# Kernel tuning notes

Hardware: AMD Instinct MI355X
Metric: run time of the kernel (lower is better)

The kernel has to match this reference:

```python
import jax, jax.numpy as jnp
import numpy as np

NODE_DIM, EDGE_DIM, HIDDEN, OUT_DIM, HEADS = 128, 64, 128, 64, 4
N_NODES, N_EDGES = 4096, 16384
EPS = 1e-8


def setup_inputs() -> dict:
    key = jax.random.key(0)
    ks = jax.random.split(key, 10)
    s = lambda *shape: 1.0 / np.sqrt(shape[-2] if len(shape) > 1 else shape[-1])
    return {
        "node_features": jax.random.normal(ks[0], (N_NODES, NODE_DIM), jnp.float32),
        "incidence_matrix": jax.random.uniform(ks[1], (N_NODES, N_EDGES), jnp.float32),
        # per-head node_transform: [H, node_dim, hidden]
        "W1": jax.random.normal(ks[2], (HEADS, NODE_DIM, HIDDEN), jnp.float32) * (1.0 / np.sqrt(NODE_DIM)),
        "b1": jnp.zeros((HEADS, HIDDEN), jnp.float32),
        # per-head attention_weight: Linear(hidden, 1) -> vector [H, hidden]
        "Wa": jax.random.normal(ks[3], (HEADS, HIDDEN), jnp.float32) * (1.0 / np.sqrt(HIDDEN)),
        "ba": jnp.zeros((HEADS,), jnp.float32),
        # per-head expand_output: [H, hidden, edge_dim]
        "W2": jax.random.normal(ks[4], (HEADS, HIDDEN, EDGE_DIM), jnp.float32) * (1.0 / np.sqrt(HIDDEN)),
        "b2": jnp.zeros((HEADS, EDGE_DIM), jnp.float32),
        # output_transform: [H*edge_dim, output_dim]
        "Wout": jax.random.normal(ks[5], (HEADS * EDGE_DIM, OUT_DIM), jnp.float32) * (1.0 / np.sqrt(HEADS * EDGE_DIM)),
        "bout": jnp.zeros((OUT_DIM,), jnp.float32),
    }


def _min_max_normalize(x):
    # per-column min-max over the edge axis (axis=-2)
    mn = jnp.min(x, axis=-2, keepdims=True)
    mx = jnp.max(x, axis=-2, keepdims=True)
    return (x - mn) / (mx - mn + EPS)


def reference(node_features, incidence_matrix, W1, b1, Wa, ba, W2, b2, Wout, bout):
    # transformed node features per head: [H, N, hidden]
    t = jnp.einsum("nd,hdk->hnk", node_features, W1) + b1[:, None, :]
    # incidence^T @ t -> masked edge features: [H, E, hidden]
    m = jnp.einsum("ne,hnk->hek", incidence_matrix, t)
    # attention scores: [H, E]
    scores = jnp.einsum("hek,hk->he", m, Wa) + ba[:, None]
    scores = jax.nn.leaky_relu(scores, negative_slope=0.2)
    # softmax over edges (dim=0 of [E,1] per head)
    coeffs = jax.nn.softmax(scores, axis=-1)  # [H, E]
    w = coeffs[:, :, None] * m  # [H, E, hidden]
    u = jnp.einsum("hek,hko->heo", w, W2) + b2[:, None, :]  # [H, E, edge_dim]
    u = _min_max_normalize(u)
    # concat heads -> [E, H*edge_dim]
    cat = jnp.transpose(u, (1, 0, 2)).reshape(N_EDGES, HEADS * EDGE_DIM)
    cat = jax.nn.relu(cat)  # dropout is identity in eval mode
    return cat @ Wout + bout  # [E, output_dim]
```

## Files before the change

### kernel.cpp

```cpp
#include <hip/hip_runtime.h>
#include <stdint.h>

#define NODES 4096
#define EDGES 16384
#define CSTR  288

typedef __attribute__((ext_vector_type(4))) float    f32x4;
typedef __attribute__((ext_vector_type(8))) short    short8;
typedef __attribute__((ext_vector_type(4))) uint32_t u32x4;
typedef __attribute__((ext_vector_type(4))) unsigned short u16x4;

__device__ __forceinline__ unsigned short f2bf(float f) {
  union { float f; uint32_t u; } v; v.f = f;
  uint32_t u = v.u;
  return (unsigned short)((u + 0x7fffu + ((u >> 16) & 1u)) >> 16);
}
__device__ __forceinline__ float bf2f(unsigned short s) {
  union { uint32_t u; float f; } v; v.u = ((uint32_t)s) << 16;
  return v.f;
}
__device__ __forceinline__ uint32_t fenc(float f) {
  uint32_t u = __float_as_uint(f);
  return (u >> 31) ? ~u : (u | 0x80000000u);
}
__device__ __forceinline__ float fdec(uint32_t k) {
  return (k & 0x80000000u) ? __uint_as_float(k ^ 0x80000000u) : __uint_as_float(~k);
}

__global__ __launch_bounds__(128) void k0_fold(
    const float* __restrict__ W1, const float* __restrict__ W2,
    const float* __restrict__ Wa, const float* __restrict__ b1,
    float* __restrict__ WeT, float* __restrict__ beff)
{
  const int h = blockIdx.x / 65, oi = blockIdx.x % 65;
  const int d = threadIdx.x;
  const float* W1r = W1 + (size_t)h * 16384 + (size_t)d * 128;
  float acc = 0.f, p;
  if (oi < 64) {
    const float* w2c = W2 + (size_t)h * 8192 + oi;
#pragma unroll 8
    for (int kc = 0; kc < 32; kc++) {
      f32x4 wv = *(const f32x4*)(W1r + kc * 4);
      acc += wv[0] * w2c[(size_t)(kc * 4 + 0) * 64];
      acc += wv[1] * w2c[(size_t)(kc * 4 + 1) * 64];
      acc += wv[2] * w2c[(size_t)(kc * 4 + 2) * 64];
      acc += wv[3] * w2c[(size_t)(kc * 4 + 3) * 64];
    }
    p = b1[h * 128 + d] * w2c[(size_t)d * 64];
  } else {
    const float* wac = Wa + h * 128;
#pragma unroll 8
    for (int kc = 0; kc < 32; kc++) {
      f32x4 wv = *(const f32x4*)(W1r + kc * 4);
      f32x4 av = *(const f32x4*)(wac + kc * 4);
      acc += wv[0] * av[0] + wv[1] * av[1] + wv[2] * av[2] + wv[3] * av[3];
    }
    p = b1[h * 128 + d] * wac[d];
  }
  WeT[(size_t)h * 9216 + (size_t)d * 72 + oi] = acc;
  for (int off = 32; off > 0; off >>= 1) p += __shfl_down(p, off, 64);
  __shared__ float r2s[2];
  if ((d & 63) == 0) r2s[d >> 6] = p;
  __syncthreads();
  if (d == 0) beff[h * 72 + oi] = r2s[0] + r2s[1];
}

__global__ __launch_bounds__(256) void k1_prep(
    const float* __restrict__ nf, const float* __restrict__ WeT,
    const float* __restrict__ beff, unsigned short* __restrict__ PqT)
{
  __shared__ float nf_s[8][132];
  const int n0 = blockIdx.x * 8;
  const int t = threadIdx.x;
  {
    int row = t >> 5, col = (t * 4) & 127;
    *(f32x4*)&nf_s[row][col] = *(const f32x4*)(nf + (size_t)(n0 + row) * 128 + col);
  }
  __syncthreads();
  const int h = t >> 6, o = t & 63;
  const float* wp = WeT + (size_t)h * 9216 + o;
  float acc[8];
  {
    float b = beff[h * 72 + o];
#pragma unroll
    for (int n = 0; n < 8; n++) acc[n] = b;
  }
  for (int dc = 0; dc < 32; dc++) {
    f32x4 nv[8];
#pragma unroll
    for (int n = 0; n < 8; n++) nv[n] = *(const f32x4*)&nf_s[n][dc * 4];
#pragma unroll
    for (int i = 0; i < 4; i++) {
      float wv = wp[(size_t)(dc * 4 + i) * 72];
#pragma unroll
      for (int n = 0; n < 8; n++) acc[n] += nv[n][i] * wv;
    }
  }
  {
    unsigned short b[8];
#pragma unroll
    for (int n = 0; n < 8; n++) b[n] = f2bf(acc[n]);
    u32x4 pk;
    pk[0] = (uint32_t)b[0] | ((uint32_t)b[1] << 16);
    pk[1] = (uint32_t)b[2] | ((uint32_t)b[3] << 16);
    pk[2] = (uint32_t)b[4] | ((uint32_t)b[5] << 16);
    pk[3] = (uint32_t)b[6] | ((uint32_t)b[7] << 16);
    *(u32x4*)(&PqT[(size_t)(h * 72 + o) * 4096 + n0]) = pk;
  }
  if (t < 32) {
    const int qh = t >> 3, qn = t & 7;
    const float* wq = WeT + (size_t)qh * 9216 + 64;
    float a = beff[qh * 72 + 64];
    for (int d = 0; d < 128; d++) a += nf_s[qn][d] * wq[(size_t)d * 72];
    unsigned short hi = f2bf(a);
    unsigned short lo = f2bf(a - bf2f(hi));
    PqT[(size_t)(qh * 72 + 64) * 4096 + n0 + qn] = hi;
    PqT[(size_t)(qh * 72 + 65) * 4096 + n0 + qn] = lo;
  }
  if (t < 96) {
    const int ph = t / 24, pr = (t / 4) % 6, pn = (t & 3) * 2;
    *(uint32_t*)&PqT[(size_t)(ph * 72 + 66 + pr) * 4096 + n0 + pn] = 0u;
  }
}

__global__ __launch_bounds__(256) void k2_gemm(
    const float* __restrict__ inc, const unsigned short* __restrict__ PqT,
    float* __restrict__ C, float* __restrict__ sbuf)
{
  __shared__ unsigned short As[64 * 64];
  __shared__ unsigned short AsLo[64 * 64];
  __shared__ unsigned short Bs[288 * 72];
  const int t = threadIdx.x;
  const int lane = t & 63, w = t >> 6;
  const int wr = w & 1, wc = w >> 1;
  const int e0 = blockIdx.x * 64;
  const int eq = t & 15, kq = t >> 4;

  f32x4 acc[2][9];
  for (int mi = 0; mi < 2; mi++)
    for (int ni = 0; ni < 9; ni++)
      acc[mi][ni] = (f32x4){0.f, 0.f, 0.f, 0.f};

  f32x4 av[4];
  u32x4 bv[9];

  auto load_tiles = [&](int ks) {
    const float* ap = inc + (size_t)(ks * 64 + kq * 4) * 16384 + e0 + eq * 4;
#pragma unroll
    for (int r = 0; r < 4; r++)
      av[r] = *(const f32x4*)(ap + (size_t)r * 16384);
#pragma unroll
    for (int j = 0; j < 9; j++) {
      int f = t + 256 * j; int c = f >> 3, q8 = f & 7;
      bv[j] = *(const u32x4*)(PqT + (size_t)c * 4096 + ks * 64 + q8 * 8);
    }
  };
  auto store_tiles = [&]() {
#pragma unroll
    for (int i = 0; i < 4; i++) {
      int e = 4 * eq + i;
      int p = ((kq >> 1) + eq + 4 * i) & 7;
      u16x4 wv, wl;
      wv[0] = f2bf(av[0][i]); wv[1] = f2bf(av[1][i]);
      wv[2] = f2bf(av[2][i]); wv[3] = f2bf(av[3][i]);
      wl[0] = f2bf(av[0][i] - bf2f(wv[0]));
      wl[1] = f2bf(av[1][i] - bf2f(wv[1]));
      wl[2] = f2bf(av[2][i] - bf2f(wv[2]));
      wl[3] = f2bf(av[3][i] - bf2f(wv[3]));
      *(u16x4*)(&As[e * 64 + p * 8 + (kq & 1) * 4]) = wv;
      *(u16x4*)(&AsLo[e * 64 + p * 8 + (kq & 1) * 4]) = wl;
    }
#pragma unroll
    for (int j = 0; j < 9; j++) {
      int f = t + 256 * j; int c = f >> 3, q8 = f & 7;
      *(u32x4*)(&Bs[c * 72 + q8 * 8]) = bv[j];
    }
  };
  auto compute = [&]() {
#pragma unroll
    for (int ksub = 0; ksub < 2; ksub++) {
      short8 afr[2], aflo[2];
      const int q = lane >> 4;
#pragma unroll
      for (int mi = 0; mi < 2; mi++) {
        int e = wr * 32 + mi * 16 + (lane & 15);
        int p = ((4 * ksub + q) + (e >> 2) + 4 * (e & 3)) & 7;
        afr[mi]  = *(const short8*)(&As[e * 64 + p * 8]);
        aflo[mi] = *(const short8*)(&AsLo[e * 64 + p * 8]);
      }
#pragma unroll
      for (int ni = 0; ni < 9; ni++) {
        int c = wc * 144 + ni * 16 + (lane & 15);
        const short8 bfr = *(const short8*)(&Bs[c * 72 + 32 * ksub + 8 * q]);
        acc[0][ni] = __builtin_amdgcn_mfma_f32_16x16x32_bf16(afr[0], bfr, acc[0][ni], 0, 0, 0);
        acc[1][ni] = __builtin_amdgcn_mfma_f32_16x16x32_bf16(afr[1], bfr, acc[1][ni], 0, 0, 0);
        if (ni == 4 || ni == 8) {
          acc[0][ni] = __builtin_amdgcn_mfma_f32_16x16x32_bf16(aflo[0], bfr, acc[0][ni], 0, 0, 0);
          acc[1][ni] = __builtin_amdgcn_mfma_f32_16x16x32_bf16(aflo[1], bfr, acc[1][ni], 0, 0, 0);
        }
      }
    }
  };

  load_tiles(0);
  for (int ks = 0; ks < 64; ks++) {
    __syncthreads();
    store_tiles();
    __syncthreads();
    if (ks < 63) load_tiles(ks + 1);
    compute();
  }

#pragma unroll
  for (int mi = 0; mi < 2; mi++)
#pragma unroll
    for (int ni = 0; ni < 9; ni++)
#pragma unroll
      for (int r = 0; r < 4; r++) {
        int e = e0 + wr * 32 + mi * 16 + (lane >> 4) * 4 + r;
        int c = wc * 144 + ni * 16 + (lane & 15);
        C[(size_t)e * CSTR + c] = acc[mi][ni][r];
      }

  const int l15 = lane & 15;
#pragma unroll
  for (int mi = 0; mi < 2; mi++)
#pragma unroll
    for (int r = 0; r < 4; r++) {
      int e = e0 + wr * 32 + mi * 16 + (lane >> 4) * 4 + r;
      {
        float v = acc[mi][4][r]; float vp = __shfl_xor(v, 1);
        if (l15 == 0) sbuf[(wc * 2 + 0) * 16384 + e] = v + vp;
      }
      {
        float v = acc[mi][8][r]; float vp = __shfl_xor(v, 1);
        if (l15 == 8) sbuf[(wc * 2 + 1) * 16384 + e] = v + vp;
      }
    }
}

__global__ __launch_bounds__(1024) void k3_softmax(
    const float* __restrict__ sbuf, const float* __restrict__ ba,
    float* __restrict__ coeff, uint32_t* __restrict__ pmn_a,
    uint32_t* __restrict__ pmx_a)
{
  const int h = blockIdx.x, t = threadIdx.x;
  if (t < 64) { pmn_a[h * 64 + t] = 0xFFFFFFFFu; pmx_a[h * 64 + t] = 0u; }
  __shared__ float red[16];
  float vals[16];
  float mx = -1e30f;
  const float bav = ba[h];
#pragma unroll
  for (int i = 0; i < 16; i++) {
    float s = sbuf[h * 16384 + t + 1024 * i] + bav;
    s = (s > 0.f) ? s : 0.2f * s;
    vals[i] = s;
    mx = fmaxf(mx, s);
  }
  for (int off = 32; off > 0; off >>= 1) mx = fmaxf(mx, __shfl_xor(mx, off, 64));
  if ((t & 63) == 0) red[t >> 6] = mx;
  __syncthreads();
  float gmx = red[0];
  for (int i = 1; i < 16; i++) gmx = fmaxf(gmx, red[i]);
  float total = 0.f;
#pragma unroll
  for (int i = 0; i < 16; i++) { vals[i] = expf(vals[i] - gmx); total += vals[i]; }
  __syncthreads();
  for (int off = 32; off > 0; off >>= 1) total += __shfl_xor(total, off, 64);
  if ((t & 63) == 0) red[t >> 6] = total;
  __syncthreads();
  float gs = 0.f;
  for (int i = 0; i < 16; i++) gs += red[i];
  float inv = 1.f / gs;
#pragma unroll
  for (int i = 0; i < 16; i++) coeff[h * 16384 + t + 1024 * i] = vals[i] * inv;
}

__global__ __launch_bounds__(256) void k4_minmax(
    const float* __restrict__ C, const float* __restrict__ coeff,
    uint32_t* __restrict__ pmn_a, uint32_t* __restrict__ pmx_a)
{
  const int t = threadIdx.x, blk = blockIdx.x;
  const int h = t >> 6, o = t & 63, c = h * 72 + o;
  const int e0 = blk * 64;
  float mn = 1e30f, mx = -1e30f;
  for (int e = 0; e < 64; e++) {
    float u = coeff[h * 16384 + e0 + e] * C[(size_t)(e0 + e) * CSTR + c];
    mn = fminf(mn, u); mx = fmaxf(mx, u);
  }
  atomicMin(&pmn_a[t], fenc(mn));
  atomicMax(&pmx_a[t], fenc(mx));
}

__global__ __launch_bounds__(256) void k5_out(
    const float* __restrict__ C, const float* __restrict__ coeff,
    const uint32_t* __restrict__ pmn_a, const uint32_t* __restrict__ pmx_a,
    const float* __restrict__ Wout, const float* __restrict__ bout,
    float* __restrict__ out)
{
  __shared__ float cat[16][256];
  const int t = threadIdx.x;
  const int e0 = blockIdx.x * 16;
  {
    const int h = t >> 6, o = t & 63, c = h * 72 + o;
    const float mn = fdec(pmn_a[t]);
    const float inv = 1.f / (fdec(pmx_a[t]) - mn + 1e-8f);
#pragma unroll
    for (int el = 0; el < 16; el++) {
      float u = coeff[h * 16384 + e0 + el] * C[(size_t)(e0 + el) * CSTR + c];
      float vn = (u - mn) * inv;
      cat[el][t] = vn > 0.f ? vn : 0.f;
    }
  }
  __syncthreads();
  {
    const int od = t & 63, eg = t >> 6;
    float b = bout[od];
    float a0 = b, a1 = b, a2 = b, a3 = b;
    for (int hc = 0; hc < 256; hc++) {
      float wv = Wout[(size_t)hc * 64 + od];
      a0 += cat[eg * 4 + 0][hc] * wv;
      a1 += cat[eg * 4 + 1][hc] * wv;
      a2 += cat[eg * 4 + 2][hc] * wv;
      a3 += cat[eg * 4 + 3][hc] * wv;
    }
    out[(size_t)(e0 + eg * 4 + 0) * 64 + od] = a0;
    out[(size_t)(e0 + eg * 4 + 1) * 64 + od] = a1;
    out[(size_t)(e0 + eg * 4 + 2) * 64 + od] = a2;
    out[(size_t)(e0 + eg * 4 + 3) * 64 + od] = a3;
  }
}

extern "C" void kernel_launch(void* const* d_in, const int* in_sizes, int n_in,
                              void* d_out, int out_size, void* d_ws, size_t ws_size,
                              hipStream_t stream) {
  const float* nf   = (const float*)d_in[0];
  const float* inc  = (const float*)d_in[1];
  const float* W1   = (const float*)d_in[2];
  const float* b1   = (const float*)d_in[3];
  const float* Wa   = (const float*)d_in[4];
  const float* ba   = (const float*)d_in[5];
  const float* W2   = (const float*)d_in[6];
  const float* Wout = (const float*)d_in[8];
  const float* bout = (const float*)d_in[9];
  float* out = (float*)d_out;

  char* ws = (char*)d_ws;
  unsigned short* PqT = (unsigned short*)(ws);
  float* C      = (float*)(ws + 2359296);
  float* coeff  = (float*)(ws + 21233664);
  float* sbuf   = (float*)(ws + 21495808);
  float* WeT    = (float*)(ws + 21757952);
  float* beff   = (float*)(ws + 21905408);
  uint32_t* pmn_a = (uint32_t*)(ws + 21909504);
  uint32_t* pmx_a = (uint32_t*)(ws + 21910528);

  k0_fold<<<260, 128, 0, stream>>>(W1, W2, Wa, b1, WeT, beff);
  k1_prep<<<512, 256, 0, stream>>>(nf, WeT, beff, PqT);
  k2_gemm<<<256, 256, 0, stream>>>(inc, PqT, C, sbuf);
  k3_softmax<<<4, 1024, 0, stream>>>(sbuf, ba, coeff, pmn_a, pmx_a);
  k4_minmax<<<256, 256, 0, stream>>>(C, coeff, pmn_a, pmx_a);
  k5_out<<<1024, 256, 0, stream>>>(C, coeff, pmn_a, pmx_a, Wout, bout, out);
}
```

Baseline: 464.4 us.

## Store edge features as compact bf16 and run output projection on MFMA

The GEMM epilogue now writes the edge-feature matrix as a dense bf16 [E,256] buffer instead of padded fp32 with stride 288. This cuts the memory traffic of the min-max and output kernels. The output projection is rewritten to use bf16 MFMA over 64-edge tiles, with a bf16 transposed copy of Wout prepared in extra blocks of the fold kernel. The node-prep kernel is reshaped to 128 threads, each computing two output columns. The change adds bf16 rounding error to the intermediate and normalized activations.

```diff
diff --git a/kernel.cpp b/kernel.cpp
--- a/kernel.cpp
+++ b/kernel.cpp
@@ -30,8 +30,24 @@
 __global__ __launch_bounds__(128) void k0_fold(
     const float* __restrict__ W1, const float* __restrict__ W2,
     const float* __restrict__ Wa, const float* __restrict__ b1,
-    float* __restrict__ WeT, float* __restrict__ beff)
-{
+    const float* __restrict__ Wout,
+    float* __restrict__ WeT, float* __restrict__ beff,
+    unsigned short* __restrict__ WoutT)
+{
+  if (blockIdx.x >= 260) {
+    int qi = (blockIdx.x - 260) * 128 + threadIdx.x;
+    if (qi < 4224) {
+      int od = qi / 66, kq = qi % 66;
+      u16x4 v;
+#pragma unroll
+      for (int j = 0; j < 4; j++) {
+        int k = kq * 4 + j;
+        v[j] = (k < 256) ? f2bf(Wout[(size_t)k * 64 + od]) : (unsigned short)0;
+      }
+      *(u16x4*)&WoutT[od * 264 + kq * 4] = v;
+    }
+    return;
+  }
   const int h = blockIdx.x / 65, oi = blockIdx.x % 65;
   const int d = threadIdx.x;
   const float* W1r = W1 + (size_t)h * 16384 + (size_t)d * 128;
@@ -65,25 +81,27 @@
   if (d == 0) beff[h * 72 + oi] = r2s[0] + r2s[1];
 }
 
-__global__ __launch_bounds__(256) void k1_prep(
+__global__ __launch_bounds__(128) void k1_prep(
     const float* __restrict__ nf, const float* __restrict__ WeT,
     const float* __restrict__ beff, unsigned short* __restrict__ PqT)
 {
   __shared__ float nf_s[8][132];
   const int n0 = blockIdx.x * 8;
   const int t = threadIdx.x;
+#pragma unroll
+  for (int i = 0; i < 2; i++) {
+    int idx = t + 128 * i;
+    int row = idx >> 5, c4 = idx & 31;
+    *(f32x4*)&nf_s[row][c4 * 4] = *(const f32x4*)(nf + (size_t)(n0 + row) * 128 + c4 * 4);
+  }
+  __syncthreads();
+  const int h = t >> 5, oo = t & 31;
+  const float* wp = WeT + (size_t)h * 9216 + oo;
+  float acc0[8], acc1[8];
   {
-    int row = t >> 5, col = (t * 4) & 127;
-    *(f32x4*)&nf_s[row][col] = *(const f32x4*)(nf + (size_t)(n0 + row) * 128 + col);
-  }
-  __syncthreads();
-  const int h = t >> 6, o = t & 63;
-  const float* wp = WeT + (size_t)h * 9216 + o;
-  float acc[8];
-  {
-    float b = beff[h * 72 + o];
-#pragma unroll
-    for (int n = 0; n < 8; n++) acc[n] = b;
+    float b0 = beff[h * 72 + oo], b1v = beff[h * 72 + oo + 32];
+#pragma unroll
+    for (int n = 0; n < 8; n++) { acc0[n] = b0; acc1[n] = b1v; }
   }
   for (int dc = 0; dc < 32; dc++) {
     f32x4 nv[8];
@@ -91,21 +109,32 @@
     for (int n = 0; n < 8; n++) nv[n] = *(const f32x4*)&nf_s[n][dc * 4];
 #pragma unroll
     for (int i = 0; i < 4; i++) {
-      float wv = wp[(size_t)(dc * 4 + i) * 72];
-#pragma unroll
-      for (int n = 0; n < 8; n++) acc[n] += nv[n][i] * wv;
+      float w0 = wp[(size_t)(dc * 4 + i) * 72];
+      float w1 = wp[(size_t)(dc * 4 + i) * 72 + 32];
+#pragma unroll
+      for (int n = 0; n < 8; n++) {
+        acc0[n] += nv[n][i] * w0;
+        acc1[n] += nv[n][i] * w1;
+      }
     }
   }
   {
     unsigned short b[8];
 #pragma unroll
-    for (int n = 0; n < 8; n++) b[n] = f2bf(acc[n]);
+    for (int n = 0; n < 8; n++) b[n] = f2bf(acc0[n]);
     u32x4 pk;
     pk[0] = (uint32_t)b[0] | ((uint32_t)b[1] << 16);
     pk[1] = (uint32_t)b[2] | ((uint32_t)b[3] << 16);
     pk[2] = (uint32_t)b[4] | ((uint32_t)b[5] << 16);
     pk[3] = (uint32_t)b[6] | ((uint32_t)b[7] << 16);
-    *(u32x4*)(&PqT[(size_t)(h * 72 + o) * 4096 + n0]) = pk;
+    *(u32x4*)(&PqT[(size_t)(h * 72 + oo) * 4096 + n0]) = pk;
+#pragma unroll
+    for (int n = 0; n < 8; n++) b[n] = f2bf(acc1[n]);
+    pk[0] = (uint32_t)b[0] | ((uint32_t)b[1] << 16);
+    pk[1] = (uint32_t)b[2] | ((uint32_t)b[3] << 16);
+    pk[2] = (uint32_t)b[4] | ((uint32_t)b[5] << 16);
+    pk[3] = (uint32_t)b[6] | ((uint32_t)b[7] << 16);
+    *(u32x4*)(&PqT[(size_t)(h * 72 + oo + 32) * 4096 + n0]) = pk;
   }
   if (t < 32) {
     const int qh = t >> 3, qn = t & 7;
@@ -125,7 +154,7 @@
 
 __global__ __launch_bounds__(256) void k2_gemm(
     const float* __restrict__ inc, const unsigned short* __restrict__ PqT,
-    float* __restrict__ C, float* __restrict__ sbuf)
+    unsigned short* __restrict__ Cb, float* __restrict__ sbuf)
 {
   __shared__ unsigned short As[64 * 64];
   __shared__ unsigned short AsLo[64 * 64];
@@ -214,13 +243,18 @@
 #pragma unroll
   for (int mi = 0; mi < 2; mi++)
 #pragma unroll
-    for (int ni = 0; ni < 9; ni++)
-#pragma unroll
-      for (int r = 0; r < 4; r++) {
-        int e = e0 + wr * 32 + mi * 16 + (lane >> 4) * 4 + r;
-        int c = wc * 144 + ni * 16 + (lane & 15);
-        C[(size_t)e * CSTR + c] = acc[mi][ni][r];
-      }
+    for (int ni = 0; ni < 9; ni++) {
+      int cl = wc * 144 + ni * 16 + (lane & 15);
+      int hl = cl / 72, o = cl - hl * 72;
+      if (o < 64) {
+        int cbcol = hl * 64 + o;
+#pragma unroll
+        for (int r = 0; r < 4; r++) {
+          int e = e0 + wr * 32 + mi * 16 + (lane >> 4) * 4 + r;
+          Cb[(size_t)e * 256 + cbcol] = f2bf(acc[mi][ni][r]);
+        }
+      }
+    }
 
   const int l15 = lane & 15;
 #pragma unroll
@@ -277,15 +311,15 @@
 }
 
 __global__ __launch_bounds__(256) void k4_minmax(
-    const float* __restrict__ C, const float* __restrict__ coeff,
+    const unsigned short* __restrict__ Cb, const float* __restrict__ coeff,
     uint32_t* __restrict__ pmn_a, uint32_t* __restrict__ pmx_a)
 {
   const int t = threadIdx.x, blk = blockIdx.x;
-  const int h = t >> 6, o = t & 63, c = h * 72 + o;
+  const int h = t >> 6;
   const int e0 = blk * 64;
   float mn = 1e30f, mx = -1e30f;
   for (int e = 0; e < 64; e++) {
-    float u = coeff[h * 16384 + e0 + e] * C[(size_t)(e0 + e) * CSTR + c];
+    float u = coeff[h * 16384 + e0 + e] * bf2f(Cb[(size_t)(e0 + e) * 256 + t]);
     mn = fminf(mn, u); mx = fmaxf(mx, u);
   }
   atomicMin(&pmn_a[t], fenc(mn));
@@ -293,41 +327,61 @@
 }
 
 __global__ __launch_bounds__(256) void k5_out(
-    const float* __restrict__ C, const float* __restrict__ coeff,
+    const unsigned short* __restrict__ Cb, const float* __restrict__ coeff,
     const uint32_t* __restrict__ pmn_a, const uint32_t* __restrict__ pmx_a,
-    const float* __restrict__ Wout, const float* __restrict__ bout,
+    const unsigned short* __restrict__ WoutT, const float* __restrict__ bout,
     float* __restrict__ out)
 {
-  __shared__ float cat[16][256];
+  __shared__ unsigned short cat_s[64 * 264];
   const int t = threadIdx.x;
-  const int e0 = blockIdx.x * 16;
-  {
-    const int h = t >> 6, o = t & 63, c = h * 72 + o;
-    const float mn = fdec(pmn_a[t]);
-    const float inv = 1.f / (fdec(pmx_a[t]) - mn + 1e-8f);
-#pragma unroll
-    for (int el = 0; el < 16; el++) {
-      float u = coeff[h * 16384 + e0 + el] * C[(size_t)(e0 + el) * CSTR + c];
-      float vn = (u - mn) * inv;
-      cat[el][t] = vn > 0.f ? vn : 0.f;
-    }
-  }
-  __syncthreads();
-  {
-    const int od = t & 63, eg = t >> 6;
-    float b = bout[od];
-    float a0 = b, a1 = b, a2 = b, a3 = b;
-    for (int hc = 0; hc < 256; hc++) {
-      float wv = Wout[(size_t)hc * 64 + od];
-      a0 += cat[eg * 4 + 0][hc] * wv;
-      a1 += cat[eg * 4 + 1][hc] * wv;
-      a2 += cat[eg * 4 + 2][hc] * wv;
-      a3 += cat[eg * 4 + 3][hc] * wv;
-    }
-    out[(size_t)(e0 + eg * 4 + 0) * 64 + od] = a0;
-    out[(size_t)(e0 + eg * 4 + 1) * 64 + od] = a1;
-    out[(size_t)(e0 + eg * 4 + 2) * 64 + od] = a2;
-    out[(size_t)(e0 + eg * 4 + 3) * 64 + od] = a3;
+  const int e0 = blockIdx.x * 64;
+  const int cq = t & 63, w64 = t >> 6;
+  float mn[4], inv[4];
+#pragma unroll
+  for (int j = 0; j < 4; j++) {
+    uint32_t a = pmn_a[cq * 4 + j], b = pmx_a[cq * 4 + j];
+    mn[j] = fdec(a);
+    inv[j] = 1.f / (fdec(b) - mn[j] + 1e-8f);
+  }
+  const int hh = cq >> 4;
+#pragma unroll
+  for (int i = 0; i < 16; i++) {
+    int e = w64 + 4 * i;
+    float cf = coeff[hh * 16384 + e0 + e];
+    u16x4 cb = *(const u16x4*)(Cb + (size_t)(e0 + e) * 256 + cq * 4);
+    unsigned short o4[4];
+#pragma unroll
+    for (int j = 0; j < 4; j++) {
+      float u = cf * bf2f(cb[j]);
+      float vn = (u - mn[j]) * inv[j];
+      vn = vn > 0.f ? vn : 0.f;
+      o4[j] = f2bf(vn);
+    }
+    u16x4 pk; pk[0] = o4[0]; pk[1] = o4[1]; pk[2] = o4[2]; pk[3] = o4[3];
+    *(u16x4*)&cat_s[e * 264 + cq * 4] = pk;
+  }
+  __syncthreads();
+  const int lane = t & 63, w = t >> 6, l15 = lane & 15, q = lane >> 4;
+  f32x4 oacc[4];
+#pragma unroll
+  for (int ni = 0; ni < 4; ni++) oacc[ni] = (f32x4){0.f, 0.f, 0.f, 0.f};
+#pragma unroll
+  for (int kstep = 0; kstep < 8; kstep++) {
+    short8 afr = *(const short8*)&cat_s[(w * 16 + l15) * 264 + kstep * 32 + q * 8];
+#pragma unroll
+    for (int ni = 0; ni < 4; ni++) {
+      short8 bfr = *(const short8*)(WoutT + (size_t)(ni * 16 + l15) * 264 + kstep * 32 + q * 8);
+      oacc[ni] = __builtin_amdgcn_mfma_f32_16x16x32_bf16(afr, bfr, oacc[ni], 0, 0, 0);
+    }
+  }
+#pragma unroll
+  for (int ni = 0; ni < 4; ni++) {
+    float bo = bout[ni * 16 + l15];
+#pragma unroll
+    for (int r = 0; r < 4; r++) {
+      int e = e0 + w * 16 + q * 4 + r;
+      out[(size_t)e * 64 + ni * 16 + l15] = oacc[ni][r] + bo;
+    }
   }
 }
 
@@ -346,19 +400,20 @@
   float* out = (float*)d_out;
 
   char* ws = (char*)d_ws;
-  unsigned short* PqT = (unsigned short*)(ws);
-  float* C      = (float*)(ws + 2359296);
-  float* coeff  = (float*)(ws + 21233664);
-  float* sbuf   = (float*)(ws + 21495808);
-  float* WeT    = (float*)(ws + 21757952);
-  float* beff   = (float*)(ws + 21905408);
-  uint32_t* pmn_a = (uint32_t*)(ws + 21909504);
-  uint32_t* pmx_a = (uint32_t*)(ws + 21910528);
-
-  k0_fold<<<260, 128, 0, stream>>>(W1, W2, Wa, b1, WeT, beff);
-  k1_prep<<<512, 256, 0, stream>>>(nf, WeT, beff, PqT);
-  k2_gemm<<<256, 256, 0, stream>>>(inc, PqT, C, sbuf);
+  unsigned short* PqT   = (unsigned short*)(ws);
+  unsigned short* Cb    = (unsigned short*)(ws + 2359296);
+  float* coeff          = (float*)(ws + 10747904);
+  float* sbuf           = (float*)(ws + 11010048);
+  float* WeT            = (float*)(ws + 11272192);
+  float* beff           = (float*)(ws + 11419648);
+  unsigned short* WoutT = (unsigned short*)(ws + 11423744);
+  uint32_t* pmn_a       = (uint32_t*)(ws + 11460608);
+  uint32_t* pmx_a       = (uint32_t*)(ws + 11464704);
+
+  k0_fold<<<293, 128, 0, stream>>>(W1, W2, Wa, b1, Wout, WeT, beff, WoutT);
+  k1_prep<<<512, 128, 0, stream>>>(nf, WeT, beff, PqT);
+  k2_gemm<<<256, 256, 0, stream>>>(inc, PqT, Cb, sbuf);
   k3_softmax<<<4, 1024, 0, stream>>>(sbuf, ba, coeff, pmn_a, pmx_a);
-  k4_minmax<<<256, 256, 0, stream>>>(C, coeff, pmn_a, pmx_a);
-  k5_out<<<1024, 256, 0, stream>>>(C, coeff, pmn_a, pmx_a, Wout, bout, out);
-}
+  k4_minmax<<<256, 256, 0, stream>>>(Cb, coeff, pmn_a, pmx_a);
+  k5_out<<<256, 256, 0, stream>>>(Cb, coeff, pmn_a, pmx_a, WoutT, bout, out);
+}
```

Measured after the change: 452.7 us. 2.5% less time.
